# Optimization experiments

Measured on AMD Instinct MI355X. Metric: run time of the kernel, lower is better.

The kernel has to match this reference:

```python
import jax, jax.numpy as jnp
import numpy as np

T, B, H, V = 256, 64, 512, 50000
SLICE = 100
NLAYERS = 2
MAX_FORGET = 0.875
HR = 23   # hidden_radix: hiddens kept in 23-bit fixed point
FR = 10   # forget-gate fixed-point radix


def _qround(x, radix):
    s = 2.0 ** radix
    return x + jax.lax.stop_gradient(jnp.round(x * s) / s - x)


def _qfloor(x, radix):
    s = 2.0 ** radix
    return x + jax.lax.stop_gradient(jnp.floor(x * s) / s - x)


def _half_update(h, z, g):
    # reversible fixed-point update: h <- floor(h * z_q) + fix((1-z)*g)
    # (remainder bits of the multiply are pushed to the InformationBuffer in
    # the original; they don't affect the forward value, only reversal)
    zq = _qfloor(z, FR)
    h = _qfloor(h * zq, HR)
    return h + _qround((1.0 - z) * g, HR)


def _cell(x, h, p):
    # RevGRU: update h1 from (x, h2), then h2 from (x, new h1)
    Wzr1, bzr1, Wg1, bg1, Wzr2, bzr2, Wg2, bg2 = p
    half = h.shape[-1] // 2
    h1, h2 = h[:, :half], h[:, half:]
    zr1 = jax.nn.sigmoid(jnp.concatenate([x, h2], -1) @ Wzr1 + bzr1)
    z1 = MAX_FORGET * zr1[:, :half] + (1.0 - MAX_FORGET)  # bounded forgetting
    r1 = zr1[:, half:]
    g1 = jnp.tanh(jnp.concatenate([x, r1 * h2], -1) @ Wg1 + bg1)
    h1 = _half_update(h1, z1, g1)
    zr2 = jax.nn.sigmoid(jnp.concatenate([x, h1], -1) @ Wzr2 + bzr2)
    z2 = MAX_FORGET * zr2[:, :half] + (1.0 - MAX_FORGET)
    r2 = zr2[:, half:]
    g2 = jnp.tanh(jnp.concatenate([x, r2 * h1], -1) @ Wg2 + bg2)
    h2 = _half_update(h2, z2, g2)
    return jnp.concatenate([h1, h2], -1)


def _forward(emb, layer_params, input_seq):
    x_seq = emb[input_seq]  # [T, B, H]
    bsz = input_seq.shape[1]
    h0 = tuple(jnp.zeros((bsz, emb.shape[1]), emb.dtype) for _ in range(NLAYERS))

    def step(carry, x):
        hs = list(carry)
        saved = hs[-1][:, :SLICE]  # top-layer slice saved BEFORE update
        cur = x
        for l in range(NLAYERS):
            hnew = _cell(cur, hs[l], layer_params[l])
            if l != NLAYERS - 1:
                cur = hnew  # output_hidden == float view of recurrent hidden
            hs[l] = hnew
        return tuple(hs), saved

    carry, saved = jax.lax.scan(step, h0, x_seq)
    saved = jnp.concatenate([saved, carry[-1][None, :, :SLICE]], 0)  # [T+1,B,slice]
    return jnp.stack(carry), saved


def setup_inputs():
    key = jax.random.key(0)
    ks = jax.random.split(key, 20)
    half = H // 2
    inp = {
        "input_seq": jax.random.randint(ks[0], (T, B), 0, V),
        "emb": jax.random.normal(ks[1], (V, H), jnp.float32) * 0.1,
    }
    i = 2
    for l in range(NLAYERS):
        for nm, (din, dout) in [("Wzr1", (H + half, H)), ("Wg1", (H + half, half)),
                                ("Wzr2", (H + half, H)), ("Wg2", (H + half, half))]:
            inp[f"{nm}_{l}"] = jax.random.normal(ks[i], (din, dout), jnp.float32) / np.sqrt(din)
            inp[f"b{nm[1:]}_{l}"] = jnp.zeros((dout,), jnp.float32)
            i += 1
    return inp


def reference(input_seq, emb,
              Wzr1_0, bzr1_0, Wg1_0, bg1_0, Wzr2_0, bzr2_0, Wg2_0, bg2_0,
              Wzr1_1, bzr1_1, Wg1_1, bg1_1, Wzr2_1, bzr2_1, Wg2_1, bg2_1):
    p0 = (Wzr1_0, bzr1_0, Wg1_0, bg1_0, Wzr2_0, bzr2_0, Wg2_0, bg2_0)
    p1 = (Wzr1_1, bzr1_1, Wg1_1, bg1_1, Wzr2_1, bzr2_1, Wg2_1, bg2_1)
    return _forward(emb, (p0, p1), input_seq)
```

## Files before the change

kernel.cpp:

```cpp
#include <hip/hip_runtime.h>
#include <hip/hip_bf16.h>
#include <stdint.h>

#define T_STEPS 256
#define BATCH   64
#define HID     512
#define HALF    256
#define NCOLS   1536
#define MROWS   (T_STEPS * BATCH)
#define SLICE_N 100
#define SAVED_OFF (2 * BATCH * HID)

#define PSLOT 2048
#define PSTEP (12 * PSLOT)

#define RING_D 32
#define NHELP 24

#define XBUF 16384
#define WG_FRAGS 6144

typedef short bf16x8 __attribute__((ext_vector_type(8)));
typedef float f32x4  __attribute__((ext_vector_type(4)));

__device__ __forceinline__ f32x4 mfma16(bf16x8 a, bf16x8 b, f32x4 c) {
  return __builtin_amdgcn_mfma_f32_16x16x32_bf16(a, b, c, 0, 0, 0);
}
__device__ __forceinline__ float sigm_f(float x) {
  return __builtin_amdgcn_rcpf(1.f + __expf(-x));
}
__device__ __forceinline__ float tanh_f(float x) {
  x = fminf(fmaxf(x, -30.f), 30.f);
  float e = __expf(-2.f * x);
  return (1.f - e) * __builtin_amdgcn_rcpf(1.f + e);
}

__device__ __forceinline__ unsigned long long coh_u64(const void* p) {
  return __hip_atomic_load((const unsigned long long*)p, __ATOMIC_RELAXED,
                           __HIP_MEMORY_SCOPE_AGENT);
}
__device__ __forceinline__ void coh_store_u64(void* p, unsigned long long v) {
  __hip_atomic_store((unsigned long long*)p, v, __ATOMIC_RELAXED,
                     __HIP_MEMORY_SCOPE_AGENT);
}
__device__ __forceinline__ bf16x8 coh_frag(const void* p) {
  union { unsigned long long u[2]; bf16x8 v; } x;
  x.u[0] = coh_u64(p);
  x.u[1] = coh_u64((const char*)p + 8);
  return x.v;
}
__device__ __forceinline__ float4 coh_f4(const void* p) {
  union { unsigned long long u[2]; float4 v; } x;
  x.u[0] = coh_u64(p);
  x.u[1] = coh_u64((const char*)p + 8);
  return x.v;
}

#define POLLGE(addr, val)                                                        \
  while (__hip_atomic_load((addr), __ATOMIC_RELAXED, __HIP_MEMORY_SCOPE_AGENT) < \
         (uint32_t)(val))                                                        \
    __builtin_amdgcn_s_sleep(1);

struct AllW {
  const float* W[8];
  const float* b[8];
};

__global__ void prep_weights(AllW aw, __hip_bfloat16* __restrict__ Wcs,
                             __hip_bfloat16* __restrict__ WxT,
                             float* __restrict__ biasAll,
                             uint32_t* __restrict__ flags) {
  int tid = blockIdx.x * blockDim.x + threadIdx.x;
  if (tid < 4096) flags[tid] = 0u;
  const int NWc = 2 * 8 * WG_FRAGS;
  const int NX = 2 * NCOLS * 64;
  if (tid < NWc) {
    int l = tid / (8 * WG_FRAGS), r = tid % (8 * WG_FRAGS);
    int j = r / WG_FRAGS, r2 = r % WG_FRAGS;
    int g = r2 >> 6, lane = r2 & 63;
    int lrow = lane & 15, lgrp = lane >> 4;
    int s, gg;
    if (g < 32)      { s = 0; gg = g; }
    else if (g < 48) { s = 1; gg = g - 32; }
    else if (g < 80) { s = 2; gg = g - 48; }
    else             { s = 3; gg = g - 80; }
    int ct = gg >> 3, kt = gg & 7;
    int zr = (s == 0 || s == 2);
    int nc = zr ? 512 : 256;
    int cb = zr ? (ct < 2 ? 32 * j + 16 * ct : 256 + 32 * j + 16 * (ct - 2))
                : (32 * j + 16 * ct);
    const float* W = aw.W[l * 4 + s];
    int kbase = 512 + kt * 32 + lgrp * 8;
    __hip_bfloat16 frag[8];
#pragma unroll
    for (int e = 0; e < 8; ++e)
      frag[e] = __float2bfloat16(W[(size_t)(kbase + e) * nc + cb + lrow]);
    *(uint4*)&Wcs[(size_t)tid * 8] = *(uint4*)frag;
  } else if (tid < NWc + NX) {
    int u = tid - NWc;
    int l = u / (NCOLS * 64), r = u % (NCOLS * 64);
    int c = r >> 6, k0 = (r & 63) * 8;
    const float* W; int nc, cc;
    if (c < 512)       { W = aw.W[l*4+0]; nc = 512; cc = c;        }
    else if (c < 768)  { W = aw.W[l*4+1]; nc = 256; cc = c - 512;  }
    else if (c < 1280) { W = aw.W[l*4+2]; nc = 512; cc = c - 768;  }
    else               { W = aw.W[l*4+3]; nc = 256; cc = c - 1280; }
    __hip_bfloat16 frag[8];
#pragma unroll
    for (int e = 0; e < 8; ++e)
      frag[e] = __float2bfloat16(W[(size_t)(k0 + e) * nc + cc]);
    *(uint4*)&WxT[((size_t)l * NCOLS + c) * 512 + k0] = *(uint4*)frag;
  } else if (tid < NWc + NX + 2 * NCOLS) {
    int c = tid - NWc - NX;
    int l = c / NCOLS, cc = c % NCOLS;
    const float* b; int off;
    if (cc < 512)       { b = aw.b[l*4+0]; off = cc;        }
    else if (cc < 768)  { b = aw.b[l*4+1]; off = cc - 512;  }
    else if (cc < 1280) { b = aw.b[l*4+2]; off = cc - 768;  }
    else                { b = aw.b[l*4+3]; off = cc - 1280; }
    biasAll[c] = b[off];
  }
}

__global__ void embed_gather(const int* __restrict__ seq, const float* __restrict__ emb,
                             __hip_bfloat16* __restrict__ X0) {
  int i = blockIdx.x * blockDim.x + threadIdx.x;
  int row = i >> 7, c4 = (i & 127) * 4;
  int idx = seq[row];
  float4 v = *(const float4*)&emb[(size_t)idx * HID + c4];
  union { __hip_bfloat16 h[4]; uint2 u; } pk;
  pk.h[0] = __float2bfloat16(v.x);
  pk.h[1] = __float2bfloat16(v.y);
  pk.h[2] = __float2bfloat16(v.z);
  pk.h[3] = __float2bfloat16(v.w);
  *(uint2*)&X0[(size_t)row * HID + c4] = pk.u;
}

__global__ __launch_bounds__(256) void gemm_p(const __hip_bfloat16* __restrict__ A,
                                              const __hip_bfloat16* __restrict__ WT,
                                              const float* __restrict__ bias,
                                              float* __restrict__ Psw) {
  const int tid = threadIdx.x;
  const int lane = tid & 63, w = tid >> 6;
  const int lrow = lane & 15, lgrp = lane >> 4;
  const int n0 = blockIdx.x * 64, m0 = blockIdx.y * 64;
  const int wm = w & 1, wn = w >> 1;
  __shared__ __hip_bfloat16 As[64][72];
  f32x4 acc[2][2];
#pragma unroll
  for (int a = 0; a < 2; ++a)
#pragma unroll
    for (int b = 0; b < 2; ++b) acc[a][b] = (f32x4){0.f, 0.f, 0.f, 0.f};

  const int lr = tid >> 2, lc = (tid & 3) * 16;
  for (int k0 = 0; k0 < 512; k0 += 64) {
    *(uint4*)&As[lr][lc]     = *(const uint4*)&A[((size_t)m0 + lr) * 512 + k0 + lc];
    *(uint4*)&As[lr][lc + 8] = *(const uint4*)&A[((size_t)m0 + lr) * 512 + k0 + lc + 8];
    __syncthreads();
#pragma unroll
    for (int kt = 0; kt < 2; ++kt) {
      bf16x8 a0 = *(const bf16x8*)&As[wm * 32 + lrow][kt * 32 + lgrp * 8];
      bf16x8 a1 = *(const bf16x8*)&As[wm * 32 + 16 + lrow][kt * 32 + lgrp * 8];
      bf16x8 b0 = *(const bf16x8*)&WT[((size_t)n0 + wn * 32 + lrow) * 512 + k0 + kt * 32 + lgrp * 8];
      bf16x8 b1 = *(const bf16x8*)&WT[((size_t)n0 + wn * 32 + 16 + lrow) * 512 + k0 + kt * 32 + lgrp * 8];
      acc[0][0] = mfma16(a0, b0, acc[0][0]);
      acc[0][1] = mfma16(a0, b1, acc[0][1]);
      acc[1][0] = mfma16(a1, b0, acc[1][0]);
      acc[1][1] = mfma16(a1, b1, acc[1][1]);
    }
    __syncthreads();
  }
  const int t = m0 >> 6;
#pragma unroll
  for (int mt = 0; mt < 2; ++mt) {
    int g = wm * 2 + mt;
#pragma unroll
    for (int nt = 0; nt < 2; ++nt) {
      int colb = n0 + wn * 32 + nt * 16;
      int slot, wt;
      if (colb < 512)       { int c = colb;        wt = (c & 255) >> 5; slot = (c >> 8) * 2 + ((c >> 4) & 1); }
      else if (colb < 768)  { int c = colb - 512;  wt = c >> 5;         slot = 4 + ((c >> 4) & 1); }
      else if (colb < 1280) { int c = colb - 768;  wt = (c & 255) >> 5; slot = 6 + (c >> 8) * 2 + ((c >> 4) & 1); }
      else                  { int c = colb - 1280; wt = c >> 5;         slot = 10 + ((c >> 4) & 1); }
      float bv = bias[colb + lrow];
      float4 v;
      v.x = acc[mt][nt][0] + bv;
      v.y = acc[mt][nt][1] + bv;
      v.z = acc[mt][nt][2] + bv;
      v.w = acc[mt][nt][3] + bv;
      size_t off = (((size_t)g * 256 + t) * 12 + slot) * PSLOT + (size_t)wt * 256 + (size_t)lane * 4;
      *(float4*)&Psw[off] = v;
    }
  }
}

struct SharedMem {
  union {
    struct {
      __hip_bfloat16 Wl[WG_FRAGS * 8];
      __hip_bfloat16 Ab[XBUF];
      __hip_bfloat16 st[2048];
      float zl[2048];
      float h1s[2048];
      float h2s[2048];
    } rec;
    struct {
      __hip_bfloat16 Bs[64][520];
      __hip_bfloat16 As[2 * XBUF];
      float bias[64];
    } hlp;
  };
};

template <int LAYER>
__device__ __forceinline__ const float* paddr(const float* Pb, int g4, int t,
                                              int slot, int j, int lane) {
  size_t tt = LAYER ? (size_t)(t & (RING_D - 1)) : (size_t)t;
  size_t TD = LAYER ? RING_D : 256;
  return Pb + (((size_t)g4 * TD + tt) * 12 + slot) * PSLOT + (size_t)j * 256 +
         (size_t)lane * 4;
}

#define AB_FILL(srcbuf)                                                      \
  {                                                                          \
    const char* sp = (const char*)(srcbuf) + (size_t)tid * 16;               \
    bf16x8 t0 = coh_frag(sp);                                                \
    bf16x8 t1 = coh_frag(sp + 8192);                                         \
    bf16x8 t2 = coh_frag(sp + 16384);                                        \
    bf16x8 t3 = coh_frag(sp + 24576);                                        \
    *(bf16x8*)&Ab[((size_t)0 * 512 + tid) * 8] = t0;                         \
    *(bf16x8*)&Ab[((size_t)1 * 512 + tid) * 8] = t1;                         \
    *(bf16x8*)&Ab[((size_t)2 * 512 + tid) * 8] = t2;                         \
    *(bf16x8*)&Ab[((size_t)3 * 512 + tid) * 8] = t3;                         \
  }

#define XCOPY(Gbase)                                                         \
  {                                                                          \
    int a_ = tid >> 7, rem_ = tid & 127, ln_ = rem_ >> 1, hf_ = rem_ & 1;    \
    unsigned long long v_ =                                                  \
        *(const unsigned long long*)&st[(a_ * 64 + ln_) * 8 + hf_ * 4];      \
    coh_store_u64(&(Gbase)[(((size_t)(a_ * 8 + j) * 64 + ln_) * 8 + hf_ * 4)], v_); \
  }

template <int LAYER>
__device__ void rec_body(const __hip_bfloat16* __restrict__ Wcs_j,
                         const float* __restrict__ Pbase,
                         __hip_bfloat16* __restrict__ R,
                         float* __restrict__ out,
                         uint32_t* __restrict__ flags,
                         SharedMem& sm, int j) {
  const int tid = threadIdx.x;
  const int lane = tid & 63, w = tid >> 6;
  const int lrow = lane & 15, lgrp = lane >> 4;

  uint32_t* F = flags + LAYER * 1024;
  uint32_t* cnt1 = flags + 2048;
  uint32_t* l1prog = flags + 2304;

  __hip_bfloat16* const Wl = sm.rec.Wl;
  __hip_bfloat16* const Ab = sm.rec.Ab;
  __hip_bfloat16* const st = sm.rec.st;
  float* const zl  = sm.rec.zl;
  float* const h1s = sm.rec.h1s;
  float* const h2s = sm.rec.h2s;

  const int HM = LAYER ? 1 : 7;
  __hip_bfloat16* const h1r = R + (size_t)(LAYER ? 20 : 0)  * XBUF;
  __hip_bfloat16* const h2r = R + (size_t)(LAYER ? 22 : 8)  * XBUF;
  __hip_bfloat16* const ag1 = R + (size_t)(LAYER ? 24 : 16) * XBUF;
  __hip_bfloat16* const ag2 = R + (size_t)(LAYER ? 26 : 18) * XBUF;

  for (int i = tid; i < WG_FRAGS; i += 512)
    *(bf16x8*)&Wl[(size_t)i * 8] = *(const bf16x8*)&Wcs_j[(size_t)i * 8];
  for (int i = tid; i < 2048; i += 512) { h1s[i] = 0.f; h2s[i] = 0.f; }
  if (LAYER == 1)
    for (int i = tid; i < 64 * 32; i += 512) {
      int row = i >> 5, c = 32 * j + (i & 31);
      if (c < SLICE_N) out[SAVED_OFF + (size_t)row * SLICE_N + c] = 0.f;
    }
  __syncthreads();

  const int ct13 = w >> 1, a0 = (w & 1) * 2, a1 = a0 + 1;
  const int cl13 = 16 * (ct13 & 1) + lrow;
  const int lt13 = (lgrp * 4) | ((cl13 >> 3) << 4);
  const int el13 = cl13 & 7;
  const int ct24 = w >> 2, a24 = w & 3;
  const int cl24 = 16 * ct24 + lrow;
  const int lt24 = (lgrp * 4) | ((cl24 >> 3) << 4);
  const int el24 = cl24 & 7;
  const int col24 = 32 * j + cl24;
  const int row24 = a24 * 16 + lgrp * 4;

  const float Q23 = 8388608.f, IQ23 = 1.f / 8388608.f;
  const float Q10 = 1024.f,    IQ10 = 1.f / 1024.f;

  float hr1[4] = {0.f, 0.f, 0.f, 0.f};
  float hr2[4] = {0.f, 0.f, 0.f, 0.f};

  for (int t = 0; t < T_STEPS; ++t) {
    auto LDP = [&](int g, int slot) -> float4 {
      const float* a = paddr<LAYER>(Pbase, g, t, slot, j, lane);
      if (LAYER == 1) return coh_f4(a);
      return *(const float4*)a;
    };
    float4 P_s1_0, P_s1_1, P_s2, P_s3_0, P_s3_1, P_s4;
    if (LAYER == 0) {
      P_s1_0 = LDP(a0, ct13);      P_s1_1 = LDP(a1, ct13);
      P_s2   = LDP(a24, 4 + ct24);
      P_s3_0 = LDP(a0, 6 + ct13);  P_s3_1 = LDP(a1, 6 + ct13);
      P_s4   = LDP(a24, 10 + ct24);
    }

    if (tid == 0) {
      if (LAYER == 1) { POLLGE(&cnt1[t], NHELP); }
      if (t > 0)      { POLLGE(&F[3 * 256 + t - 1], 8); }
    }
    __syncthreads();
    if (LAYER == 1) {
      P_s1_0 = LDP(a0, ct13);      P_s1_1 = LDP(a1, ct13);
      P_s2   = LDP(a24, 4 + ct24);
      P_s3_0 = LDP(a0, 6 + ct13);  P_s3_1 = LDP(a1, 6 + ct13);
      P_s4   = LDP(a24, 10 + ct24);
    }
    if (t == 0) {
      bf16x8 zz = {0, 0, 0, 0, 0, 0, 0, 0};
#pragma unroll
      for (int q = 0; q < 4; ++q) *(bf16x8*)&Ab[((size_t)q * 512 + tid) * 8] = zz;
    } else {
      AB_FILL(&h2r[(size_t)((t - 1) & HM) * XBUF]);
    }
    __syncthreads();
    {
      f32x4 c0 = (f32x4){0.f, 0.f, 0.f, 0.f}, c1 = c0;
#pragma unroll
      for (int kt = 0; kt < 8; ++kt) {
        bf16x8 A0 = *(const bf16x8*)&Ab[((a0 * 8 + kt) * 64 + lane) * 8];
        bf16x8 A1 = *(const bf16x8*)&Ab[((a1 * 8 + kt) * 64 + lane) * 8];
        bf16x8 B  = *(const bf16x8*)&Wl[((ct13 * 8 + kt) * 64 + lane) * 8];
        c0 = mfma16(A0, B, c0);
        c1 = mfma16(A1, B, c1);
      }
      if (ct13 < 2) {
#pragma unroll
        for (int rr = 0; rr < 4; ++rr) {
          zl[(a0 * 16 + lgrp * 4 + rr) * 32 + cl13] = 0.875f * sigm_f(c0[rr] + P_s1_0[rr]) + 0.125f;
          zl[(a1 * 16 + lgrp * 4 + rr) * 32 + cl13] = 0.875f * sigm_f(c1[rr] + P_s1_1[rr]) + 0.125f;
        }
      } else {
#pragma unroll
        for (int rr = 0; rr < 4; ++rr) {
          float r0 = sigm_f(c0[rr] + P_s1_0[rr]);
          float r1 = sigm_f(c1[rr] + P_s1_1[rr]);
          st[(a0 * 64 + lt13 + rr) * 8 + el13] =
              __float2bfloat16(r0 * h2s[(a0 * 16 + lgrp * 4 + rr) * 32 + cl13]);
          st[(a1 * 64 + lt13 + rr) * 8 + el13] =
              __float2bfloat16(r1 * h2s[(a1 * 16 + lgrp * 4 + rr) * 32 + cl13]);
        }
      }
    }
    __syncthreads();
    XCOPY(&ag1[(size_t)(t & 1) * XBUF]);
    __syncthreads();
    if (tid == 0)
      __hip_atomic_fetch_add(&F[0 * 256 + t], 1u, __ATOMIC_RELAXED, __HIP_MEMORY_SCOPE_AGENT);

    if (tid == 0) {
      POLLGE(&F[0 * 256 + t], 8);
      if (LAYER == 0 && t >= 8) { POLLGE(&cnt1[t - 8], NHELP); }
    }
    __syncthreads();
    AB_FILL(&ag1[(size_t)(t & 1) * XBUF]);
    __syncthreads();
    {
      f32x4 c = (f32x4){0.f, 0.f, 0.f, 0.f};
#pragma unroll
      for (int kt = 0; kt < 8; ++kt) {
        bf16x8 A = *(const bf16x8*)&Ab[((a24 * 8 + kt) * 64 + lane) * 8];
        bf16x8 B = *(const bf16x8*)&Wl[((32 + ct24 * 8 + kt) * 64 + lane) * 8];
        c = mfma16(A, B, c);
      }
#pragma unroll
      for (int rr = 0; rr < 4; ++rr) {
        float gv = tanh_f(c[rr] + P_s2[rr]);
        float z  = zl[(row24 + rr) * 32 + cl24];
        float zq = floorf(z * Q10) * IQ10;
        float h = hr1[rr];
        h = floorf(h * zq * Q23) * IQ23;
        h = h + rintf((1.f - z) * gv * Q23) * IQ23;
        hr1[rr] = h;
        h1s[(row24 + rr) * 32 + cl24] = h;
        st[(a24 * 64 + lt24 + rr) * 8 + el24] = __float2bfloat16(h);
        int row = row24 + rr;
        if (LAYER == 1 && col24 < SLICE_N)
          out[SAVED_OFF + (size_t)(t + 1) * (BATCH * SLICE_N) + (size_t)row * SLICE_N + col24] = h;
        if (t == T_STEPS - 1)
          out[(size_t)LAYER * (BATCH * HID) + (size_t)row * HID + col24] = h;
      }
    }
    __syncthreads();
    XCOPY(&h1r[(size_t)(t & HM) * XBUF]);
    __syncthreads();
    if (tid == 0)
      __hip_atomic_fetch_add(&F[1 * 256 + t], 1u, __ATOMIC_RELAXED, __HIP_MEMORY_SCOPE_AGENT);

    if (tid == 0) { POLLGE(&F[1 * 256 + t], 8); }
    __syncthreads();
    AB_FILL(&h1r[(size_t)(t & HM) * XBUF]);
    __syncthreads();
    {
      f32x4 c0 = (f32x4){0.f, 0.f, 0.f, 0.f}, c1 = c0;
#pragma unroll
      for (int kt = 0; kt < 8; ++kt) {
        bf16x8 A0 = *(const bf16x8*)&Ab[((a0 * 8 + kt) * 64 + lane) * 8];
        bf16x8 A1 = *(const bf16x8*)&Ab[((a1 * 8 + kt) * 64 + lane) * 8];
        bf16x8 B  = *(const bf16x8*)&Wl[((48 + ct13 * 8 + kt) * 64 + lane) * 8];
        c0 = mfma16(A0, B, c0);
        c1 = mfma16(A1, B, c1);
      }
      if (ct13 < 2) {
#pragma unroll
        for (int rr = 0; rr < 4; ++rr) {
          zl[(a0 * 16 + lgrp * 4 + rr) * 32 + cl13] = 0.875f * sigm_f(c0[rr] + P_s3_0[rr]) + 0.125f;
          zl[(a1 * 16 + lgrp * 4 + rr) * 32 + cl13] = 0.875f * sigm_f(c1[rr] + P_s3_1[rr]) + 0.125f;
        }
      } else {
#pragma unroll
        for (int rr = 0; rr < 4; ++rr) {
          float r0 = sigm_f(c0[rr] + P_s3_0[rr]);
          float r1 = sigm_f(c1[rr] + P_s3_1[rr]);
          st[(a0 * 64 + lt13 + rr) * 8 + el13] =
              __float2bfloat16(r0 * h1s[(a0 * 16 + lgrp * 4 + rr) * 32 + cl13]);
          st[(a1 * 64 + lt13 + rr) * 8 + el13] =
              __float2bfloat16(r1 * h1s[(a1 * 16 + lgrp * 4 + rr) * 32 + cl13]);
        }
      }
    }
    __syncthreads();
    XCOPY(&ag2[(size_t)(t & 1) * XBUF]);
    __syncthreads();
    if (tid == 0)
      __hip_atomic_fetch_add(&F[2 * 256 + t], 1u, __ATOMIC_RELAXED, __HIP_MEMORY_SCOPE_AGENT);

    if (tid == 0) { POLLGE(&F[2 * 256 + t], 8); }
    __syncthreads();
    AB_FILL(&ag2[(size_t)(t & 1) * XBUF]);
    __syncthreads();
    {
      f32x4 c = (f32x4){0.f, 0.f, 0.f, 0.f};
#pragma unroll
      for (int kt = 0; kt < 8; ++kt) {
        bf16x8 A = *(const bf16x8*)&Ab[((a24 * 8 + kt) * 64 + lane) * 8];
        bf16x8 B = *(const bf16x8*)&Wl[((80 + ct24 * 8 + kt) * 64 + lane) * 8];
        c = mfma16(A, B, c);
      }
#pragma unroll
      for (int rr = 0; rr < 4; ++rr) {
        float gv = tanh_f(c[rr] + P_s4[rr]);
        float z  = zl[(row24 + rr) * 32 + cl24];
        float zq = floorf(z * Q10) * IQ10;
        float h = hr2[rr];
        h = floorf(h * zq * Q23) * IQ23;
        h = h + rintf((1.f - z) * gv * Q23) * IQ23;
        hr2[rr] = h;
        h2s[(row24 + rr) * 32 + cl24] = h;
        st[(a24 * 64 + lt24 + rr) * 8 + el24] = __float2bfloat16(h);
        int row = row24 + rr;
        if (t == T_STEPS - 1)
          out[(size_t)LAYER * (BATCH * HID) + (size_t)row * HID + HALF + col24] = h;
      }
    }
    __syncthreads();
    XCOPY(&h2r[(size_t)(t & HM) * XBUF]);
    __syncthreads();
    if (tid == 0) {
      __hip_atomic_fetch_add(&F[3 * 256 + t], 1u, __ATOMIC_RELAXED, __HIP_MEMORY_SCOPE_AGENT);
      if (LAYER == 1)
        __hip_atomic_store(&l1prog[j], (uint32_t)(t + 1), __ATOMIC_RELAXED, __HIP_MEMORY_SCOPE_AGENT);
    }
  }
}

__device__ void helper_body(const __hip_bfloat16* __restrict__ WxT1,
                            const float* __restrict__ bias1,
                            const __hip_bfloat16* __restrict__ R,
                            float* __restrict__ P1ring,
                            uint32_t* __restrict__ flags,
                            SharedMem& sm, int n) {
  const int tid = threadIdx.x;
  const int lane = tid & 63, w = tid >> 6;
  const int lrow = lane & 15, lgrp = lane >> 4;
  const int n0 = n * 64;

  uint32_t* F0 = flags;
  uint32_t* cnt1 = flags + 2048;
  uint32_t* l1prog = flags + 2304;
  const __hip_bfloat16* h1r = R;
  const __hip_bfloat16* h2r = R + (size_t)8 * XBUF;

  for (int i = tid; i < 64 * 64; i += 512) {
    int c = i >> 6, k8 = (i & 63) * 8;
    *(bf16x8*)&sm.hlp.Bs[c][k8] = *(const bf16x8*)&WxT1[(size_t)(n0 + c) * 512 + k8];
  }
  if (tid < 64) sm.hlp.bias[tid] = bias1[n0 + tid];
  __syncthreads();

  const int mt = w & 3, chb = (w >> 2) * 2;

  for (int t = 0; t < T_STEPS; ++t) {
    if (tid == 0) {
      POLLGE(&F0[3 * 256 + t], 8);
      if (t >= RING_D) {
        for (;;) {
          uint32_t mm = 0xffffffffu;
#pragma unroll
          for (int q = 0; q < 8; ++q) {
            uint32_t v = __hip_atomic_load(&l1prog[q], __ATOMIC_RELAXED, __HIP_MEMORY_SCOPE_AGENT);
            mm = v < mm ? v : mm;
          }
          if (mm + (uint32_t)(RING_D - 1) >= (uint32_t)t) break;
          __builtin_amdgcn_s_sleep(1);
        }
      }
    }
    __syncthreads();
    {
      const char* s1 = (const char*)&h1r[(size_t)(t & 7) * XBUF] + (size_t)tid * 16;
      const char* s2 = (const char*)&h2r[(size_t)(t & 7) * XBUF] + (size_t)tid * 16;
      bf16x8 tA[8];
#pragma unroll
      for (int k = 0; k < 4; ++k) tA[k] = coh_frag(s1 + (size_t)k * 8192);
#pragma unroll
      for (int k = 4; k < 8; ++k) tA[k] = coh_frag(s2 + (size_t)(k - 4) * 8192);
#pragma unroll
      for (int k = 0; k < 8; ++k) *(bf16x8*)&sm.hlp.As[(size_t)(k * 512 + tid) * 8] = tA[k];
    }
    __syncthreads();
#pragma unroll
    for (int q = 0; q < 2; ++q) {
      int ch = chb + q;
      f32x4 c = (f32x4){0.f, 0.f, 0.f, 0.f};
#pragma unroll
      for (int kt = 0; kt < 16; ++kt) {
        const bf16x8 A = *(const bf16x8*)&sm.hlp.As[
            kt < 8 ? (size_t)((mt * 8 + kt) * 64 + lane) * 8
                   : (size_t)XBUF + (size_t)((mt * 8 + (kt - 8)) * 64 + lane) * 8];
        const bf16x8 B = *(const bf16x8*)&sm.hlp.Bs[ch * 16 + lrow][kt * 32 + lgrp * 8];
        c = mfma16(A, B, c);
      }
      int colb = n0 + ch * 16;
      int slot, wt;
      if (colb < 512)       { int cc = colb;        wt = (cc & 255) >> 5; slot = (cc >> 8) * 2 + ((cc >> 4) & 1); }
      else if (colb < 768)  { int cc = colb - 512;  wt = cc >> 5;         slot = 4 + ((cc >> 4) & 1); }
      else if (colb < 1280) { int cc = colb - 768;  wt = (cc & 255) >> 5; slot = 6 + (cc >> 8) * 2 + ((cc >> 4) & 1); }
      else                  { int cc = colb - 1280; wt = cc >> 5;         slot = 10 + ((cc >> 4) & 1); }
      float bv = sm.hlp.bias[ch * 16 + lrow];
      union { float4 f; unsigned long long u[2]; } uv;
      uv.f.x = c[0] + bv; uv.f.y = c[1] + bv; uv.f.z = c[2] + bv; uv.f.w = c[3] + bv;
      size_t off = (((size_t)mt * RING_D + (t & (RING_D - 1))) * 12 + slot) * PSLOT +
                   (size_t)wt * 256 + (size_t)lane * 4;
      unsigned long long* d = (unsigned long long*)&P1ring[off];
      coh_store_u64(d, uv.u[0]);
      coh_store_u64(d + 1, uv.u[1]);
    }
    __syncthreads();
    if (tid == 0)
      __hip_atomic_fetch_add(&cnt1[t], 1u, __ATOMIC_RELAXED, __HIP_MEMORY_SCOPE_AGENT);
  }
}

__global__ __attribute__((amdgpu_waves_per_eu(2))) __launch_bounds__(512)
void fused_kernel(const __hip_bfloat16* __restrict__ Wcs,
                  const float* __restrict__ Psw0,
                  float* __restrict__ P1ring,
                  const __hip_bfloat16* __restrict__ WxT1,
                  const float* __restrict__ bias1,
                  float* __restrict__ out,
                  __hip_bfloat16* __restrict__ R,
                  uint32_t* __restrict__ flags) {
  __shared__ SharedMem sm;
  const int bid = blockIdx.x;
  if (bid < 8)
    rec_body<0>(Wcs + (size_t)bid * WG_FRAGS * 8, Psw0, R, out, flags, sm, bid);
  else if (bid < 16)
    rec_body<1>(Wcs + (size_t)(8 + (bid - 8)) * WG_FRAGS * 8, P1ring, R, out, flags, sm, bid - 8);
  else
    helper_body(WxT1, bias1, R, P1ring, flags, sm, bid - 16);
}

extern "C" void kernel_launch(void* const* d_in, const int* in_sizes, int n_in,
                              void* d_out, int out_size, void* d_ws, size_t ws_size,
                              hipStream_t stream) {
  const int*   seq = (const int*)d_in[0];
  const float* emb = (const float*)d_in[1];
  AllW aw;
  for (int l = 0; l < 2; ++l)
    for (int s = 0; s < 4; ++s) {
      aw.W[l * 4 + s] = (const float*)d_in[2 + l * 8 + s * 2];
      aw.b[l * 4 + s] = (const float*)d_in[2 + l * 8 + s * 2 + 1];
    }

  uint8_t* wp = (uint8_t*)d_ws;
  float* Psw = (float*)wp;                   wp += (size_t)4 * 256 * PSTEP * 4;
  __hip_bfloat16* X0 = (__hip_bfloat16*)wp;  wp += (size_t)MROWS * HID * 2;
  __hip_bfloat16* R  = (__hip_bfloat16*)wp;  wp += (size_t)MROWS * HID * 2;
  __hip_bfloat16* Wcs = (__hip_bfloat16*)wp; wp += (size_t)2 * 8 * WG_FRAGS * 8 * 2;
  __hip_bfloat16* WxT = (__hip_bfloat16*)wp; wp += (size_t)2 * NCOLS * 512 * 2;
  float* biasAll = (float*)wp;               wp += (size_t)2 * NCOLS * 4;
  uint32_t* flags = (uint32_t*)wp;           wp += 16384;

  float* out = (float*)d_out;

  const int prepTot = 2 * 8 * WG_FRAGS + 2 * NCOLS * 64 + 2 * NCOLS;
  const int prepN = (prepTot + 255) / 256;
  prep_weights<<<prepN, 256, 0, stream>>>(aw, Wcs, WxT, biasAll, flags);
  embed_gather<<<(MROWS * 128) / 256, 256, 0, stream>>>(seq, emb, X0);

  gemm_p<<<dim3(24, 256), 256, 0, stream>>>(X0, WxT, biasAll, Psw);
  fused_kernel<<<8 + 8 + NHELP, 512, 0, stream>>>(
      Wcs, Psw, (float*)X0, WxT + (size_t)NCOLS * 512, biasAll + NCOLS,
      out, R, flags);
}
```

Baseline: 3.083 ms.

## Replace block-wide barriers with per-wave flag signaling in recurrent kernel

```diff
diff --git a/kernel.cpp b/kernel.cpp
--- a/kernel.cpp
+++ b/kernel.cpp
@@ -60,6 +60,9 @@
   while (__hip_atomic_load((addr), __ATOMIC_RELAXED, __HIP_MEMORY_SCOPE_AGENT) < \
          (uint32_t)(val))                                                        \
     __builtin_amdgcn_s_sleep(1);
+
+#define CFENCE() asm volatile("" ::: "memory")
+#define WAVE_VM() asm volatile("s_waitcnt vmcnt(0)" ::: "memory")
 
 struct AllW {
   const float* W[8];
@@ -203,6 +206,7 @@
       float zl[2048];
       float h1s[2048];
       float h2s[2048];
+      uint32_t fcnt[8];
     } rec;
     struct {
       __hip_bfloat16 Bs[64][520];
@@ -234,12 +238,15 @@
     *(bf16x8*)&Ab[((size_t)3 * 512 + tid) * 8] = t3;                         \
   }
 
-#define XCOPY(Gbase)                                                         \
-  {                                                                          \
-    int a_ = tid >> 7, rem_ = tid & 127, ln_ = rem_ >> 1, hf_ = rem_ & 1;    \
-    unsigned long long v_ =                                                  \
-        *(const unsigned long long*)&st[(a_ * 64 + ln_) * 8 + hf_ * 4];      \
-    coh_store_u64(&(Gbase)[(((size_t)(a_ * 8 + j) * 64 + ln_) * 8 + hf_ * 4)], v_); \
+#define WAVE_FLAG(sidx, gflag)                                               \
+  if (lane == 0) {                                                           \
+    int sl_ = ((unsigned)t * 4 + (sidx)) & 7;                                \
+    uint32_t old_ = atomicAdd(&fcnt[sl_], 1u);                               \
+    if (old_ == 7) {                                                         \
+      fcnt[sl_] = 0;                                                         \
+      __hip_atomic_fetch_add((gflag), 1u, __ATOMIC_RELAXED,                  \
+                             __HIP_MEMORY_SCOPE_AGENT);                      \
+    }                                                                        \
   }
 
 template <int LAYER>
@@ -263,6 +270,7 @@
   float* const zl  = sm.rec.zl;
   float* const h1s = sm.rec.h1s;
   float* const h2s = sm.rec.h2s;
+  uint32_t* const fcnt = sm.rec.fcnt;
 
   const int HM = LAYER ? 1 : 7;
   __hip_bfloat16* const h1r = R + (size_t)(LAYER ? 20 : 0)  * XBUF;
@@ -273,6 +281,7 @@
   for (int i = tid; i < WG_FRAGS; i += 512)
     *(bf16x8*)&Wl[(size_t)i * 8] = *(const bf16x8*)&Wcs_j[(size_t)i * 8];
   for (int i = tid; i < 2048; i += 512) { h1s[i] = 0.f; h2s[i] = 0.f; }
+  if (tid < 8) fcnt[tid] = 0u;
   if (LAYER == 1)
     for (int i = tid; i < 64 * 32; i += 512) {
       int row = i >> 5, c = 32 * j + (i & 31);
@@ -290,6 +299,9 @@
   const int el24 = cl24 & 7;
   const int col24 = 32 * j + cl24;
   const int row24 = a24 * 16 + lgrp * 4;
+  const int pu = lane >> 1, phf = (lane & 1) * 4;
+  const int plt13 = (ct13 & 1) * 32 + pu;
+  const int plt24 = ct24 * 32 + pu;
 
   const float Q23 = 8388608.f, IQ23 = 1.f / 8388608.f;
   const float Q10 = 1024.f,    IQ10 = 1.f / 1024.f;
@@ -311,11 +323,13 @@
       P_s4   = LDP(a24, 10 + ct24);
     }
 
-    if (tid == 0) {
+    if (lane == 0) {
       if (LAYER == 1) { POLLGE(&cnt1[t], NHELP); }
       if (t > 0)      { POLLGE(&F[3 * 256 + t - 1], 8); }
-    }
-    __syncthreads();
+      if (LAYER == 1 && tid == 0 && t > 0)
+        __hip_atomic_store(&l1prog[j], (uint32_t)t, __ATOMIC_RELAXED, __HIP_MEMORY_SCOPE_AGENT);
+    }
+    CFENCE();
     if (LAYER == 1) {
       P_s1_0 = LDP(a0, ct13);      P_s1_1 = LDP(a1, ct13);
       P_s2   = LDP(a24, 4 + ct24);
@@ -356,19 +370,22 @@
           st[(a1 * 64 + lt13 + rr) * 8 + el13] =
               __float2bfloat16(r1 * h2s[(a1 * 16 + lgrp * 4 + rr) * 32 + cl13]);
         }
-      }
-    }
-    __syncthreads();
-    XCOPY(&ag1[(size_t)(t & 1) * XBUF]);
-    __syncthreads();
-    if (tid == 0)
-      __hip_atomic_fetch_add(&F[0 * 256 + t], 1u, __ATOMIC_RELAXED, __HIP_MEMORY_SCOPE_AGENT);
-
-    if (tid == 0) {
+        CFENCE();
+        __hip_bfloat16* dst = &ag1[(size_t)(t & 1) * XBUF];
+        unsigned long long v0 = *(const unsigned long long*)&st[(a0 * 64 + plt13) * 8 + phf];
+        unsigned long long v1 = *(const unsigned long long*)&st[(a1 * 64 + plt13) * 8 + phf];
+        coh_store_u64(&dst[((size_t)(a0 * 8 + j) * 64 + plt13) * 8 + phf], v0);
+        coh_store_u64(&dst[((size_t)(a1 * 8 + j) * 64 + plt13) * 8 + phf], v1);
+        WAVE_VM();
+      }
+    }
+    WAVE_FLAG(0, &F[0 * 256 + t]);
+
+    if (lane == 0) {
       POLLGE(&F[0 * 256 + t], 8);
       if (LAYER == 0 && t >= 8) { POLLGE(&cnt1[t - 8], NHELP); }
     }
-    __syncthreads();
+    CFENCE();
     AB_FILL(&ag1[(size_t)(t & 1) * XBUF]);
     __syncthreads();
     {
@@ -396,15 +413,16 @@
         if (t == T_STEPS - 1)
           out[(size_t)LAYER * (BATCH * HID) + (size_t)row * HID + col24] = h;
       }
-    }
-    __syncthreads();
-    XCOPY(&h1r[(size_t)(t & HM) * XBUF]);
-    __syncthreads();
-    if (tid == 0)
-      __hip_atomic_fetch_add(&F[1 * 256 + t], 1u, __ATOMIC_RELAXED, __HIP_MEMORY_SCOPE_AGENT);
-
-    if (tid == 0) { POLLGE(&F[1 * 256 + t], 8); }
-    __syncthreads();
+      CFENCE();
+      __hip_bfloat16* dst = &h1r[(size_t)(t & HM) * XBUF];
+      unsigned long long v = *(const unsigned long long*)&st[(a24 * 64 + plt24) * 8 + phf];
+      coh_store_u64(&dst[((size_t)(a24 * 8 + j) * 64 + plt24) * 8 + phf], v);
+      WAVE_VM();
+    }
+    WAVE_FLAG(1, &F[1 * 256 + t]);
+
+    if (lane == 0) { POLLGE(&F[1 * 256 + t], 8); }
+    CFENCE();
     AB_FILL(&h1r[(size_t)(t & HM) * XBUF]);
     __syncthreads();
     {
@@ -433,16 +451,19 @@
           st[(a1 * 64 + lt13 + rr) * 8 + el13] =
               __float2bfloat16(r1 * h1s[(a1 * 16 + lgrp * 4 + rr) * 32 + cl13]);
         }
-      }
-    }
-    __syncthreads();
-    XCOPY(&ag2[(size_t)(t & 1) * XBUF]);
-    __syncthreads();
-    if (tid == 0)
-      __hip_atomic_fetch_add(&F[2 * 256 + t], 1u, __ATOMIC_RELAXED, __HIP_MEMORY_SCOPE_AGENT);
-
-    if (tid == 0) { POLLGE(&F[2 * 256 + t], 8); }
-    __syncthreads();
+        CFENCE();
+        __hip_bfloat16* dst = &ag2[(size_t)(t & 1) * XBUF];
+        unsigned long long v0 = *(const unsigned long long*)&st[(a0 * 64 + plt13) * 8 + phf];
+        unsigned long long v1 = *(const unsigned long long*)&st[(a1 * 64 + plt13) * 8 + phf];
+        coh_store_u64(&dst[((size_t)(a0 * 8 + j) * 64 + plt13) * 8 + phf], v0);
+        coh_store_u64(&dst[((size_t)(a1 * 8 + j) * 64 + plt13) * 8 + phf], v1);
+        WAVE_VM();
+      }
+    }
+    WAVE_FLAG(2, &F[2 * 256 + t]);
+
+    if (lane == 0) { POLLGE(&F[2 * 256 + t], 8); }
+    CFENCE();
     AB_FILL(&ag2[(size_t)(t & 1) * XBUF]);
     __syncthreads();
     {
@@ -468,15 +489,13 @@
         if (t == T_STEPS - 1)
           out[(size_t)LAYER * (BATCH * HID) + (size_t)row * HID + HALF + col24] = h;
       }
-    }
-    __syncthreads();
-    XCOPY(&h2r[(size_t)(t & HM) * XBUF]);
-    __syncthreads();
-    if (tid == 0) {
-      __hip_atomic_fetch_add(&F[3 * 256 + t], 1u, __ATOMIC_RELAXED, __HIP_MEMORY_SCOPE_AGENT);
-      if (LAYER == 1)
-        __hip_atomic_store(&l1prog[j], (uint32_t)(t + 1), __ATOMIC_RELAXED, __HIP_MEMORY_SCOPE_AGENT);
-    }
+      CFENCE();
+      __hip_bfloat16* dst = &h2r[(size_t)(t & HM) * XBUF];
+      unsigned long long v = *(const unsigned long long*)&st[(a24 * 64 + plt24) * 8 + phf];
+      coh_store_u64(&dst[((size_t)(a24 * 8 + j) * 64 + plt24) * 8 + phf], v);
+      WAVE_VM();
+    }
+    WAVE_FLAG(3, &F[3 * 256 + t]);
   }
 }
 
@@ -507,7 +526,7 @@
   const int mt = w & 3, chb = (w >> 2) * 2;
 
   for (int t = 0; t < T_STEPS; ++t) {
-    if (tid == 0) {
+    if (lane == 0) {
       POLLGE(&F0[3 * 256 + t], 8);
       if (t >= RING_D) {
         for (;;) {
@@ -522,7 +541,7 @@
         }
       }
     }
-    __syncthreads();
+    CFENCE();
     {
       const char* s1 = (const char*)&h1r[(size_t)(t & 7) * XBUF] + (size_t)tid * 16;
       const char* s2 = (const char*)&h2r[(size_t)(t & 7) * XBUF] + (size_t)tid * 16;
```

After: 3.920 ms. 1.27x slower.
